# Kernel optimization log

Measured on AMD Instinct MI355X. Metric: run time of the kernel, lower is better.

## Reference

```python
import jax, jax.numpy as jnp
import numpy as np

B, S, H, L, NH, DH, V, FF, WD, W = 16, 512, 768, 12, 12, 64, 30522, 3072, 256, 255
T = S - 1


def layer_norm(x, s, b, eps=1e-12):
    m = jnp.mean(x, -1, keepdims=True)
    v = jnp.mean((x - m) ** 2, -1, keepdims=True)
    return (x - m) * jax.lax.rsqrt(v + eps) * s + b


def setup_inputs() -> dict:
    key = jax.random.key(0)
    ks = jax.random.split(key, 20)
    rng = np.random.RandomState(0)
    # ragged structure: words per sentence and wordpieces per word
    sent_lens = rng.randint(128, W + 1, size=B)
    token_lens = np.zeros((B, W), dtype=np.int32)
    for i in range(B):
        token_lens[i, : sent_lens[i]] = rng.randint(1, 3, size=sent_lens[i])
    bert_len = token_lens.sum(1)  # wordpieces per sentence (no CLS/SEP)
    attention_mask = (np.arange(S)[None, :] < (bert_len + 2)[:, None]).astype(np.int32)
    input_ids = rng.randint(0, V, size=(B, S)).astype(np.int32)
    sd = 0.02
    rn = lambda k, sh: jax.random.normal(k, sh, jnp.float32) * sd
    inp = {
        "input_ids": jnp.asarray(input_ids),
        "attention_mask": jnp.asarray(attention_mask),
        "token_lens": jnp.asarray(token_lens),
        "word_emb": rn(ks[0], (V, H)),
        "pos_emb": rn(ks[1], (S, H)),
        "type_emb": rn(ks[2], (2, H)),
        "emb_ln_s": jnp.ones((H,), jnp.float32),
        "emb_ln_b": jnp.zeros((H,), jnp.float32),
        "Wq": rn(ks[3], (L, H, H)), "bq": jnp.zeros((L, H), jnp.float32),
        "Wk": rn(ks[4], (L, H, H)), "bk": jnp.zeros((L, H), jnp.float32),
        "Wv": rn(ks[5], (L, H, H)), "bv": jnp.zeros((L, H), jnp.float32),
        "Wo": rn(ks[6], (L, H, H)), "bo": jnp.zeros((L, H), jnp.float32),
        "ln1_s": jnp.ones((L, H), jnp.float32), "ln1_b": jnp.zeros((L, H), jnp.float32),
        "W1": rn(ks[7], (L, H, FF)), "b1": jnp.zeros((L, FF), jnp.float32),
        "W2": rn(ks[8], (L, FF, H)), "b2": jnp.zeros((L, H), jnp.float32),
        "ln2_s": jnp.ones((L, H), jnp.float32), "ln2_b": jnp.zeros((L, H), jnp.float32),
        "proj_W": rn(ks[9], (H, WD)), "proj_b": jnp.zeros((WD,), jnp.float32),
    }
    return inp


def reference(input_ids, attention_mask, token_lens, word_emb, pos_emb, type_emb,
              emb_ln_s, emb_ln_b, Wq, bq, Wk, bk, Wv, bv, Wo, bo, ln1_s, ln1_b,
              W1, b1, W2, b2, ln2_s, ln2_b, proj_W, proj_b):
    # --- BERT embeddings ---
    h = word_emb[input_ids] + pos_emb[None, :, :] + type_emb[0][None, None, :]
    h = layer_norm(h, emb_ln_s, emb_ln_b)
    att_bias = (1.0 - attention_mask.astype(jnp.float32))[:, None, None, :] * -10000.0

    def block(h, p):
        wq, bq_, wk, bk_, wv, bv_, wo, bo_, l1s, l1b, w1, b1_, w2, b2_, l2s, l2b = p
        q = (h @ wq + bq_).reshape(B, S, NH, DH)
        k = (h @ wk + bk_).reshape(B, S, NH, DH)
        v = (h @ wv + bv_).reshape(B, S, NH, DH)
        scores = jnp.einsum('bqnd,bknd->bnqk', q, k) / np.float32(np.sqrt(DH)) + att_bias
        a = jax.nn.softmax(scores, axis=-1)
        ctx = jnp.einsum('bnqk,bknd->bqnd', a, v).reshape(B, S, H)
        h = layer_norm(h + ctx @ wo + bo_, l1s, l1b)
        f = jax.nn.gelu(h @ w1 + b1_, approximate=False) @ w2 + b2_
        h = layer_norm(h + f, l2s, l2b)
        return h, None

    h, _ = jax.lax.scan(block, h, (Wq, bq, Wk, bk, Wv, bv, Wo, bo, ln1_s, ln1_b,
                                   W1, b1, W2, b2, ln2_s, ln2_b))
    # drop [CLS], project to word_dims
    hid = h[:, 1:, :] @ proj_W + proj_b  # [B, T, WD]
    # --- ragged segment-mean merge (vectorized form of merge_embedding) ---
    cum = jnp.cumsum(token_lens, axis=1)  # [B, W]
    pos = jnp.arange(T)
    word_id = jnp.sum(pos[None, :, None] >= cum[:, None, :], axis=-1)  # token -> word
    valid = pos[None, :] < cum[:, -1][:, None]  # token within bert_len
    onehot = ((word_id[:, :, None] == jnp.arange(W)[None, None, :]) & valid[:, :, None]).astype(hid.dtype)
    sums = jnp.einsum('btw,btd->bwd', onehot, hid)  # [B, W, WD]
    means = sums / jnp.maximum(token_lens, 1)[:, :, None].astype(hid.dtype)
    word_masks = (token_lens > 0).astype(jnp.float32)  # [B, W]
    return means, word_masks
```

## Files before the change

### kernel.cpp

```cpp
#include <hip/hip_runtime.h>
#include <stdint.h>

#define B_ 16
#define S_ 512
#define H_ 768
#define L_ 12
#define NH_ 12
#define DH_ 64
#define FF_ 3072
#define WD_ 256
#define W_ 255
#define MTOK_ (B_*S_)
#define QKVN_ 2304
#define MPADR_ 128

typedef _Float16 f16;
typedef _Float16 f16x8 __attribute__((ext_vector_type(8)));
typedef _Float16 f16x4 __attribute__((ext_vector_type(4)));
typedef _Float16 f16x2 __attribute__((ext_vector_type(2)));
typedef float f32x4 __attribute__((ext_vector_type(4)));

#define SCHED_FENCE() __builtin_amdgcn_sched_barrier(0)

__device__ __forceinline__ float gelu_fast(float x) {
  float u = x * (1.0f + 0.044715f * x * x);
  float e = __expf(-1.5957691216f * u);
  return __fdividef(x, 1.0f + e);
}

__device__ __forceinline__ void gload16(const f16* g, f16* l) {
  __builtin_amdgcn_global_load_lds(
      (const __attribute__((address_space(1))) void*)g,
      (__attribute__((address_space(3))) void*)l, 16, 0, 0);
}

template<int BM, int BN, int ACT, int OUTF16, int BIAS, int QKVW, int SPLITK, int CIN, int COUT>
__global__ __launch_bounds__(256) void gemm2_k(
    const f16* __restrict__ A, const f16* __restrict__ Bm, void* __restrict__ Cv,
    const float* __restrict__ bias, f16* __restrict__ vTp,
    const int* __restrict__ rowmap, const int* __restrict__ meta,
    int lda, int ldb, int ldc, int K, float scale, long czoff)
{
  constexpr int MI = BM / 32;
  constexpr int NI = BN / 32;
  const int gx = gridDim.x;
  int flat = blockIdx.y * gx + blockIdx.x;
  const int nlive = (meta[1] / BM) * gx;
  if (flat >= nlive) return;
  {
    int q = nlive >> 3, r = nlive & 7;
    int xcd = flat & 7, idx = flat >> 3;
    flat = (xcd < r ? xcd * (q + 1) : r * (q + 1) + (xcd - r) * q) + idx;
  }
  const int row0 = (flat / gx) * BM;
  const int col0 = (flat % gx) * BN;
  const int z = (SPLITK > 1) ? blockIdx.z : 0;
  const int kc_len = K / SPLITK;
  A  += (size_t)z * kc_len;
  Bm += (size_t)z * kc_len;

  __shared__ __align__(16) f16 lA[BM * 64];
  __shared__ __align__(16) f16 lB[BN * 64];
  const int lane = threadIdx.x & 63;
  const int wave = threadIdx.x >> 6;
  const int wr = wave >> 1, wc = wave & 1;
  const int srow = lane >> 3;
  const int scol = lane & 7;
  const int cs = scol ^ srow;

  int arow[BM / 32];
#pragma unroll
  for (int i = 0; i < BM / 32; ++i) {
    int cr = row0 + (wave * (BM / 32) + i) * 8 + srow;
    arow[i] = CIN ? cr : rowmap[cr];
  }

  f32x4 acc[MI][NI] = {};
  const int nt = kc_len >> 6;
  const int rl = lane & 15, g = lane >> 4;
  for (int t = 0; t < nt; ++t) {
    __syncthreads();
    const int k0 = t * 64;
#pragma unroll
    for (int i = 0; i < BM / 32; ++i) {
      int seg = wave * (BM / 32) + i;
      gload16(&A[(size_t)arow[i] * lda + k0 + cs * 8], &lA[seg * 512]);
    }
#pragma unroll
    for (int i = 0; i < BN / 32; ++i) {
      int seg = wave * (BN / 32) + i;
      gload16(&Bm[(size_t)(col0 + seg * 8 + srow) * ldb + k0 + cs * 8], &lB[seg * 512]);
    }
    __syncthreads();
#pragma unroll
    for (int c = 0; c < 2; ++c) {
      f16x8 af[MI], bf[NI];
#pragma unroll
      for (int mi = 0; mi < MI; ++mi) {
        int r = wr * (MI * 16) + mi * 16 + rl;
        int u = (c * 4 + g) ^ (r & 7);
        af[mi] = *(const f16x8*)&lA[r * 64 + u * 8];
      }
#pragma unroll
      for (int ni = 0; ni < NI; ++ni) {
        int r = wc * (NI * 16) + ni * 16 + rl;
        int u = (c * 4 + g) ^ (r & 7);
        bf[ni] = *(const f16x8*)&lB[r * 64 + u * 8];
      }
#pragma unroll
      for (int mi = 0; mi < MI; ++mi)
#pragma unroll
        for (int ni = 0; ni < NI; ++ni)
          acc[mi][ni] = __builtin_amdgcn_mfma_f32_16x16x32_f16(af[mi], bf[ni], acc[mi][ni], 0, 0, 0);
    }
  }
  const int cl = lane & 15;
  const int rq = (lane >> 4) * 4;
#pragma unroll
  for (int mi = 0; mi < MI; ++mi) {
    const int crow0 = row0 + wr * (MI * 16) + mi * 16 + rq;
    int rows[4];
    bool contig;
    if constexpr (COUT && !QKVW) {
#pragma unroll
      for (int r = 0; r < 4; ++r) rows[r] = crow0 + r;
      contig = true;
    } else {
      const int4 rm4 = *(const int4*)&rowmap[crow0];
      rows[0] = rm4.x; rows[1] = rm4.y; rows[2] = rm4.z; rows[3] = rm4.w;
      contig = (rm4.w == rm4.x + 3) && ((rm4.x & 3) == 0);
    }
    (void)contig;
#pragma unroll
    for (int ni = 0; ni < NI; ++ni) {
      int col = col0 + wc * (NI * 16) + ni * 16 + cl;
      float bv = 0.f;
      if constexpr (BIAS) { if (SPLITK == 1 || z == 0) bv = bias[col]; }
      if constexpr (QKVW) {
        if (col >= 2 * H_) {
          int vc = col - 2 * H_;
          int h = vc >> 6, d = vc & 63;
          if (contig) {
            if (rows[0] < MTOK_) {
              int b = rows[0] >> 9, s = rows[0] & (S_ - 1);
              f16x4 o4;
#pragma unroll
              for (int r = 0; r < 4; ++r) o4[r] = (f16)(acc[mi][ni][r] * scale + bv);
              *(f16x4*)&vTp[(((size_t)(b * NH_ + h)) * DH_ + d) * S_ + s] = o4;
            }
          } else {
#pragma unroll
            for (int r = 0; r < 4; ++r) {
              int orow = rows[r];
              if (orow < MTOK_) {
                int b = orow >> 9, s = orow & (S_ - 1);
                vTp[(((size_t)(b * NH_ + h)) * DH_ + d) * S_ + s] = (f16)(acc[mi][ni][r] * scale + bv);
              }
            }
          }
          continue;
        }
      }
#pragma unroll
      for (int r = 0; r < 4; ++r) {
        float v = acc[mi][ni][r] * scale + bv;
        if constexpr (ACT == 1) v = gelu_fast(v);
        if constexpr (OUTF16) {
          ((f16*)Cv + (size_t)z * czoff)[(size_t)rows[r] * ldc + col] = (f16)v;
        } else {
          ((float*)Cv)[(size_t)rows[r] * ldc + col] = v;
        }
      }
    }
  }
}

__global__ __launch_bounds__(256) void fattn_k(
    const f16* __restrict__ qkv, const f16* __restrict__ vT,
    f16* __restrict__ ctx, const int* __restrict__ lenp)
{
  const int bh = blockIdx.x, qt = blockIdx.y;
  const int b = bh / NH_, h = bh - b * NH_;
  const int L = lenp[b];
  if ((qt << 6) >= L) return;
  const int nkt = (L + 63) >> 6;
  const int lane = threadIdx.x & 63, wave = threadIdx.x >> 6;
  const int rl = lane & 15, g = lane >> 4;
  const int srow = lane >> 3, scol = lane & 7;
  const int cs = scol ^ srow;

  __shared__ __align__(16) f16 lK[2][64 * 64];
  __shared__ __align__(16) f16 lV[2][64 * 64];
  __shared__ __align__(16) f16 lP[64 * 72];

  auto stage = [&](int p, int kt) {
#pragma unroll
    for (int i = 0; i < 2; ++i) {
      int seg = wave * 2 + i;
      int r = seg * 8 + srow;
      gload16(&qkv[((size_t)b * S_ + kt * 64 + r) * QKVN_ + H_ + h * DH_ + cs * 8], &lK[p][seg * 512]);
      gload16(&vT[((size_t)bh * DH_ + r) * S_ + kt * 64 + cs * 8], &lV[p][seg * 512]);
    }
  };

  const size_t qrow0 = (size_t)b * S_ + qt * 64 + wave * 16;
  f16x8 qf[2];
#pragma unroll
  for (int kc = 0; kc < 2; ++kc) {
    qf[kc] = *(const f16x8*)&qkv[(qrow0 + rl) * QKVN_ + h * DH_ + kc * 32 + g * 8];
    qf[kc] *= (f16)0.125f;
  }

  float lsum = 0.f;
  f32x4 accO[4] = {};

  stage(0, 0);
  for (int kt = 0; kt < nkt; ++kt) {
    if (kt + 1 < nkt) {
      stage((kt + 1) & 1, kt + 1);
      asm volatile("s_waitcnt vmcnt(4) lgkmcnt(0)" ::: "memory");
    } else {
      asm volatile("s_waitcnt vmcnt(0) lgkmcnt(0)" ::: "memory");
    }
    SCHED_FENCE();
    __builtin_amdgcn_s_barrier();
    SCHED_FENCE();
    const int p = kt & 1;

    f32x4 accS[4] = {};
    __builtin_amdgcn_s_setprio(1);
#pragma unroll
    for (int kc = 0; kc < 2; ++kc) {
#pragma unroll
      for (int ak = 0; ak < 4; ++ak) {
        int row = ak * 16 + rl;
        int u = (kc * 4 + g) ^ (row & 7);
        f16x8 kf = *(const f16x8*)&lK[p][row * 64 + u * 8];
        accS[ak] = __builtin_amdgcn_mfma_f32_16x16x32_f16(kf, qf[kc], accS[ak], 0, 0, 0);
      }
    }
    __builtin_amdgcn_s_setprio(0);

    const int kvb = kt * 64 + g * 4;
    {
      float pv[16];
      float ps = 0.f;
#pragma unroll
      for (int ak = 0; ak < 4; ++ak)
#pragma unroll
        for (int r = 0; r < 4; ++r) {
          float pp = (kvb + ak * 16 + r < L) ? __expf(accS[ak][r]) : 0.f;
          pv[ak * 4 + r] = pp;
          ps += pp;
        }
      ps += __shfl_xor(ps, 16);
      ps += __shfl_xor(ps, 32);
      lsum += ps;
      const int qrow = wave * 16 + rl;
#pragma unroll
      for (int ak = 0; ak < 4; ++ak)
#pragma unroll
        for (int r2 = 0; r2 < 2; ++r2) {
          f16x2 pk = { (f16)pv[ak * 4 + r2 * 2], (f16)pv[ak * 4 + r2 * 2 + 1] };
          *(f16x2*)&lP[qrow * 72 + ak * 16 + g * 4 + r2 * 2] = pk;
        }
    }
    __builtin_amdgcn_s_setprio(1);
#pragma unroll
    for (int kc = 0; kc < 2; ++kc) {
      f16x8 pa = *(const f16x8*)&lP[(wave * 16 + rl) * 72 + kc * 32 + g * 8];
      f16x8 vf[4];
#pragma unroll
      for (int bd = 0; bd < 4; ++bd) {
        int vrow = bd * 16 + rl;
        int u = (kc * 4 + g) ^ (vrow & 7);
        vf[bd] = *(const f16x8*)&lV[p][vrow * 64 + u * 8];
      }
#pragma unroll
      for (int bd = 0; bd < 4; ++bd)
        accO[bd] = __builtin_amdgcn_mfma_f32_16x16x32_f16(pa, vf[bd], accO[bd], 0, 0, 0);
    }
    __builtin_amdgcn_s_setprio(0);
    SCHED_FENCE();
    asm volatile("s_waitcnt lgkmcnt(0)" ::: "memory");
    SCHED_FENCE();
    __builtin_amdgcn_s_barrier();
    SCHED_FENCE();
  }

  float linv = 1.f / lsum;
  const size_t orow0 = (size_t)b * S_ + qt * 64 + wave * 16;
#pragma unroll
  for (int r = 0; r < 4; ++r) {
    float li = __shfl(linv, (lane & 48) | (g * 4 + r));
    int q = g * 4 + r;
#pragma unroll
    for (int bd = 0; bd < 4; ++bd)
      ctx[(orow0 + q) * H_ + h * DH_ + bd * 16 + rl] = (f16)(accO[bd][r] * li);
  }
}

template<typename TI>
__global__ __launch_bounds__(256) void transpose_f16_k(
    const TI* __restrict__ in, f16* __restrict__ out,
    int ldin, int ldout, long i1, long o1)
{
  const int z = blockIdx.z;
  in  += (size_t)z * i1;
  out += (size_t)z * o1;
  __shared__ float t[32][33];
  const int kt = blockIdx.y * 32, nt = blockIdx.x * 32;
  const int tx = threadIdx.x & 31, tg = threadIdx.x >> 5;
#pragma unroll
  for (int i = 0; i < 4; ++i) {
    int k = tg * 4 + i;
    t[k][tx] = (float)in[(size_t)(kt + k) * ldin + nt + tx];
  }
  __syncthreads();
#pragma unroll
  for (int i = 0; i < 4; ++i) {
    int n = tg * 4 + i;
    out[(size_t)(nt + n) * ldout + kt + tx] = (f16)t[tx][n];
  }
}

__global__ void bias_cat_k(const float* __restrict__ bq, const float* __restrict__ bk,
                           const float* __restrict__ bv, float* __restrict__ out) {
  const int l = blockIdx.y;
  const int j = blockIdx.x * 256 + threadIdx.x;
  float v = (j < H_) ? bq[l * H_ + j] : (j < 2 * H_) ? bk[l * H_ + j - H_] : bv[l * H_ + j - 2 * H_];
  out[l * QKVN_ + j] = v;
}

__global__ __launch_bounds__(256) void embed_ln_k(
    const int* __restrict__ ids, const float* __restrict__ wemb,
    const float* __restrict__ pemb, const float* __restrict__ temb,
    const float* __restrict__ lns, const float* __restrict__ lnb,
    f16* __restrict__ h16)
{
  const int row = blockIdx.x * 4 + (threadIdx.x >> 6);
  const int lane = threadIdx.x & 63;
  const int s = row & (S_ - 1);
  const float4* wp = (const float4*)(wemb + (size_t)ids[row] * H_);
  const float4* pp = (const float4*)(pemb + (size_t)s * H_);
  const float4* tp = (const float4*)temb;
  float4 x[3]; float sm = 0.f, sq = 0.f;
#pragma unroll
  for (int j = 0; j < 3; ++j) {
    int i4 = lane + 64 * j;
    float4 a = wp[i4], bb = pp[i4], c = tp[i4];
    float4 v; v.x = a.x + bb.x + c.x; v.y = a.y + bb.y + c.y;
    v.z = a.z + bb.z + c.z; v.w = a.w + bb.w + c.w;
    x[j] = v;
    sm += v.x + v.y + v.z + v.w;
    sq += v.x * v.x + v.y * v.y + v.z * v.z + v.w * v.w;
  }
#pragma unroll
  for (int o = 32; o > 0; o >>= 1) { sm += __shfl_xor(sm, o); sq += __shfl_xor(sq, o); }
  float mean = sm * (1.f / H_);
  float inv = rsqrtf(sq * (1.f / H_) - mean * mean + 1e-12f);
  f16* ho = h16 + (size_t)row * H_;
#pragma unroll
  for (int j = 0; j < 3; ++j) {
    int i4 = lane + 64 * j;
    float4 sc = ((const float4*)lns)[i4], bi = ((const float4*)lnb)[i4];
    float4 v = x[j];
    f16x4 o4 = {(f16)((v.x - mean) * inv * sc.x + bi.x),
                (f16)((v.y - mean) * inv * sc.y + bi.y),
                (f16)((v.z - mean) * inv * sc.z + bi.z),
                (f16)((v.w - mean) * inv * sc.w + bi.w)};
    *(f16x4*)&ho[i4 * 4] = o4;
  }
}

__global__ __launch_bounds__(256) void ln_res_k(
    f16* __restrict__ h16, const f16* __restrict__ tmpA, const f16* __restrict__ tmpB,
    const float* __restrict__ lns, const float* __restrict__ lnb,
    const int* __restrict__ rowmap, const int* __restrict__ meta)
{
  const int crow = blockIdx.x * 4 + (threadIdx.x >> 6);
  if (crow >= meta[0]) return;
  const int row = rowmap[crow];
  const int lane = threadIdx.x & 63;
  const f16x4* hp = (const f16x4*)(h16 + (size_t)row * H_);
  const f16x4* ta = (const f16x4*)(tmpA + (size_t)crow * H_);
  const f16x4* tb = (const f16x4*)(tmpB + (size_t)crow * H_);
  float4 x[3]; float sm = 0.f, sq = 0.f;
#pragma unroll
  for (int j = 0; j < 3; ++j) {
    int i4 = lane + 64 * j;
    f16x4 a = hp[i4], va = ta[i4], vb = tb[i4];
    float4 v;
    v.x = (float)a[0] + (float)va[0] + (float)vb[0];
    v.y = (float)a[1] + (float)va[1] + (float)vb[1];
    v.z = (float)a[2] + (float)va[2] + (float)vb[2];
    v.w = (float)a[3] + (float)va[3] + (float)vb[3];
    x[j] = v;
    sm += v.x + v.y + v.z + v.w;
    sq += v.x * v.x + v.y * v.y + v.z * v.z + v.w * v.w;
  }
#pragma unroll
  for (int o = 32; o > 0; o >>= 1) { sm += __shfl_xor(sm, o); sq += __shfl_xor(sq, o); }
  float mean = sm * (1.f / H_);
  float inv = rsqrtf(sq * (1.f / H_) - mean * mean + 1e-12f);
  f16* ho = h16 + (size_t)row * H_;
#pragma unroll
  for (int j = 0; j < 3; ++j) {
    int i4 = lane + 64 * j;
    float4 sc = ((const float4*)lns)[i4], bi = ((const float4*)lnb)[i4];
    float4 v = x[j];
    f16x4 o4 = {(f16)((v.x - mean) * inv * sc.x + bi.x),
                (f16)((v.y - mean) * inv * sc.y + bi.y),
                (f16)((v.z - mean) * inv * sc.z + bi.z),
                (f16)((v.w - mean) * inv * sc.w + bi.w)};
    *(f16x4*)&ho[i4 * 4] = o4;
  }
}

__global__ void lenmap_k(const int* __restrict__ mask, int* __restrict__ len,
                         int* __restrict__ meta, int* __restrict__ rowmap) {
  const int t = threadIdx.x;
  __shared__ int red[512];
  __shared__ int cum[17];
  const int b = t >> 5, sl = t & 31;
  int part = 0;
#pragma unroll
  for (int j = 0; j < 16; ++j) part += mask[b * S_ + sl + 32 * j];
  red[t] = part; __syncthreads();
  for (int o = 16; o > 0; o >>= 1) {
    if (sl < o) red[t] += red[t + o];
    __syncthreads();
  }
  if (t == 0) {
    int c = 0; cum[0] = 0;
    for (int bb = 0; bb < B_; ++bb) { len[bb] = red[bb * 32]; c += red[bb * 32]; cum[bb + 1] = c; }
    meta[0] = c;
    meta[1] = (c + 127) & ~127;
  }
  __syncthreads();
  const int Mv = cum[16];
  for (int i = t; i < MTOK_ + MPADR_; i += 512) {
    int orig;
    if (i < Mv) {
      int bb = 0;
#pragma unroll
      for (int k = 1; k <= 16; ++k) bb += (i >= cum[k]) ? 1 : 0;
      orig = bb * S_ + (i - cum[bb]);
    } else {
      int d = i - Mv;
      orig = MTOK_ + (d < MPADR_ ? d : MPADR_ - 1);
    }
    rowmap[i] = orig;
  }
}

__global__ __launch_bounds__(256) void merge_k(
    const f16* __restrict__ proj, const int* __restrict__ tl,
    float* __restrict__ means, float* __restrict__ masks)
{
  const int w = blockIdx.x, b = blockIdx.y;
  const int t = threadIdx.x;
  __shared__ int red[256];
  int part = 0;
  for (int j = t; j < w; j += 256) part += tl[b * W_ + j];
  red[t] = part; __syncthreads();
  for (int o = 128; o > 0; o >>= 1) { if (t < o) red[t] += red[t + o]; __syncthreads(); }
  const int start = red[0];
  const int len = tl[b * W_ + w];
  float s = 0.f;
  for (int l = 0; l < len; ++l)
    s += (float)proj[((size_t)b * S_ + 1 + start + l) * WD_ + t];
  means[((size_t)b * W_ + w) * WD_ + t] = (len > 0) ? s / (float)len : 0.f;
  if (t == 0) masks[b * W_ + w] = (len > 0) ? 1.f : 0.f;
}

extern "C" void kernel_launch(void* const* d_in, const int* in_sizes, int n_in,
                              void* d_out, int out_size, void* d_ws, size_t ws_size,
                              hipStream_t stream)
{
  (void)in_sizes; (void)n_in; (void)out_size;
  const int*   ids   = (const int*)d_in[0];
  const int*   amask = (const int*)d_in[1];
  const int*   tlens = (const int*)d_in[2];
  const float* wemb  = (const float*)d_in[3];
  const float* pemb  = (const float*)d_in[4];
  const float* temb  = (const float*)d_in[5];
  const float* elns  = (const float*)d_in[6];
  const float* elnb  = (const float*)d_in[7];
  const float* Wq = (const float*)d_in[8];  const float* bq = (const float*)d_in[9];
  const float* Wk = (const float*)d_in[10]; const float* bk = (const float*)d_in[11];
  const float* Wv = (const float*)d_in[12]; const float* bv = (const float*)d_in[13];
  const float* Wo = (const float*)d_in[14]; const float* bo = (const float*)d_in[15];
  const float* l1s = (const float*)d_in[16]; const float* l1b = (const float*)d_in[17];
  const float* W1 = (const float*)d_in[18]; const float* b1 = (const float*)d_in[19];
  const float* W2 = (const float*)d_in[20]; const float* b2 = (const float*)d_in[21];
  const float* l2s = (const float*)d_in[22]; const float* l2b = (const float*)d_in[23];
  const float* pW = (const float*)d_in[24]; const float* pb = (const float*)d_in[25];

  const int MR = MTOK_ + MPADR_;
  char* ws = (char*)d_ws;
  size_t off = 0;
  auto alloc = [&](size_t n) { void* r = ws + off; off += (n + 255) & ~(size_t)255; return r; };
  f16*   h16   = (f16*)alloc((size_t)MR * H_ * 2);
  f16*   qkv   = (f16*)alloc((size_t)MR * QKVN_ * 2);
  f16*   ctx16 = (f16*)alloc((size_t)MR * H_ * 2);
  f16*   vT    = (f16*)alloc((size_t)B_ * NH_ * DH_ * S_ * 2);
  f16*   ff16  = (f16*)alloc((size_t)MR * FF_ * 2);
  f16*   tmp16 = (f16*)alloc((size_t)MR * H_ * 2 * 2);
  f16*   projf = (f16*)alloc((size_t)MR * WD_ * 2);
  f16*   pwT   = (f16*)alloc((size_t)WD_ * H_ * 2);
  float* bqkv  = (float*)alloc((size_t)L_ * QKVN_ * 4);
  int*   lenb  = (int*)alloc(256);
  int*   meta  = (int*)alloc(256);
  int*   rowmap = (int*)alloc((size_t)MR * 4);
  f16*   tmp16b = tmp16 + (size_t)MR * H_;

  const size_t wqkv_sz = (size_t)QKVN_ * H_ * 2;
  const size_t wo_sz   = (size_t)H_ * H_ * 2;
  const size_t w1_sz   = (size_t)H_ * FF_ * 2;
  const size_t w2_sz   = (size_t)FF_ * H_ * 2;
  const size_t per_layer_w = wqkv_sz + wo_sz + w1_sz + w2_sz;
  const bool big = ws_size >= off + (size_t)L_ * per_layer_w + 8192;
  const int nz = big ? L_ : 1;
  f16* wqkv0 = (f16*)alloc((size_t)nz * wqkv_sz);
  f16* wo0   = (f16*)alloc((size_t)nz * wo_sz);
  f16* w10   = (f16*)alloc((size_t)nz * w1_sz);
  f16* w20   = (f16*)alloc((size_t)nz * w2_sz);

  lenmap_k<<<1, 512, 0, stream>>>(amask, lenb, meta, rowmap);
  embed_ln_k<<<MTOK_ / 4, 256, 0, stream>>>(ids, wemb, pemb, temb, elns, elnb, h16);
  transpose_f16_k<float><<<dim3(WD_/32, H_/32, 1), 256, 0, stream>>>(pW, pwT, WD_, H_, 0, 0);
  bias_cat_k<<<dim3(QKVN_/256, L_), 256, 0, stream>>>(bq, bk, bv, bqkv);

  if (big) {
    transpose_f16_k<float><<<dim3(H_/32, H_/32, L_), 256, 0, stream>>>(
        Wq, wqkv0,                   H_, H_, (long)H_*H_, (long)QKVN_*H_);
    transpose_f16_k<float><<<dim3(H_/32, H_/32, L_), 256, 0, stream>>>(
        Wk, wqkv0 + (size_t)H_*H_,   H_, H_, (long)H_*H_, (long)QKVN_*H_);
    transpose_f16_k<float><<<dim3(H_/32, H_/32, L_), 256, 0, stream>>>(
        Wv, wqkv0 + (size_t)2*H_*H_, H_, H_, (long)H_*H_, (long)QKVN_*H_);
    transpose_f16_k<float><<<dim3(H_/32, H_/32, L_), 256, 0, stream>>>(
        Wo, wo0, H_, H_, (long)H_*H_, (long)H_*H_);
    transpose_f16_k<float><<<dim3(FF_/32, H_/32, L_), 256, 0, stream>>>(
        W1, w10, FF_, H_, (long)H_*FF_, (long)H_*FF_);
    transpose_f16_k<float><<<dim3(H_/32, FF_/32, L_), 256, 0, stream>>>(
        W2, w20, H_, FF_, (long)FF_*H_, (long)FF_*H_);
  }

  for (int l = 0; l < L_; ++l) {
    f16* wqkv_l = wqkv0 + (size_t)(big ? l : 0) * QKVN_ * H_;
    f16* wo_l   = wo0   + (size_t)(big ? l : 0) * H_ * H_;
    f16* w1_l   = w10   + (size_t)(big ? l : 0) * H_ * FF_;
    f16* w2_l   = w20   + (size_t)(big ? l : 0) * FF_ * H_;
    if (!big) {
      transpose_f16_k<float><<<dim3(H_/32, H_/32, 1), 256, 0, stream>>>(
          Wq + (size_t)l*H_*H_, wqkv_l,                   H_, H_, 0, 0);
      transpose_f16_k<float><<<dim3(H_/32, H_/32, 1), 256, 0, stream>>>(
          Wk + (size_t)l*H_*H_, wqkv_l + (size_t)H_*H_,   H_, H_, 0, 0);
      transpose_f16_k<float><<<dim3(H_/32, H_/32, 1), 256, 0, stream>>>(
          Wv + (size_t)l*H_*H_, wqkv_l + (size_t)2*H_*H_, H_, H_, 0, 0);
      transpose_f16_k<float><<<dim3(H_/32, H_/32, 1), 256, 0, stream>>>(
          Wo + (size_t)l*H_*H_, wo_l, H_, H_, 0, 0);
      transpose_f16_k<float><<<dim3(FF_/32, H_/32, 1), 256, 0, stream>>>(
          W1 + (size_t)l*H_*FF_, w1_l, FF_, H_, 0, 0);
      transpose_f16_k<float><<<dim3(H_/32, FF_/32, 1), 256, 0, stream>>>(
          W2 + (size_t)l*FF_*H_, w2_l, H_, FF_, 0, 0);
    }
    gemm2_k<128,128,0,1,1,1,1,0,0><<<dim3(QKVN_/128, MTOK_/128, 1), 256, 0, stream>>>(
        h16, wqkv_l, qkv, bqkv + (size_t)l*QKVN_, vT, rowmap, meta, H_, H_, QKVN_, H_, 1.0f, 0);
    fattn_k<<<dim3(B_*NH_, S_/64), 256, 0, stream>>>(qkv, vT, ctx16, lenb);
    gemm2_k<64,64,0,1,1,0,2,0,1><<<dim3(H_/64, MTOK_/64, 2), 256, 0, stream>>>(
        ctx16, wo_l, tmp16, bo + (size_t)l*H_, nullptr, rowmap, meta, H_, H_, H_, H_, 1.0f, (long)MR * H_);
    ln_res_k<<<MTOK_/4, 256, 0, stream>>>(h16, tmp16, tmp16b, l1s + (size_t)l*H_, l1b + (size_t)l*H_, rowmap, meta);
    gemm2_k<128,128,1,1,1,0,1,0,1><<<dim3(FF_/128, MTOK_/128, 1), 256, 0, stream>>>(
        h16, w1_l, ff16, b1 + (size_t)l*FF_, nullptr, rowmap, meta, H_, H_, FF_, H_, 1.0f, 0);
    gemm2_k<64,64,0,1,1,0,2,1,1><<<dim3(H_/64, MTOK_/64, 2), 256, 0, stream>>>(
        ff16, w2_l, tmp16, b2 + (size_t)l*H_, nullptr, rowmap, meta, FF_, FF_, H_, FF_, 1.0f, (long)MR * H_);
    ln_res_k<<<MTOK_/4, 256, 0, stream>>>(h16, tmp16, tmp16b, l2s + (size_t)l*H_, l2b + (size_t)l*H_, rowmap, meta);
  }

  gemm2_k<64,64,0,1,1,0,1,0,0><<<dim3(WD_/64, MTOK_/64, 1), 256, 0, stream>>>(
      h16, pwT, projf, pb, nullptr, rowmap, meta, H_, H_, WD_, H_, 1.0f, 0);
  merge_k<<<dim3(W_, B_), 256, 0, stream>>>(projf, tlens,
      (float*)d_out, (float*)d_out + (size_t)B_ * W_ * WD_);
}
```

Before: 2.259 ms.

## Keep hidden states in compacted row layout across all layer kernels

Hidden states are now stored in compacted (valid-token-only) row order from the embedding onward, rather than in the padded B*S layout with a rowmap gather. GEMMs switch to a template mode that reads A rows contiguously, attention scatters its output through a new cmap into compacted rows, and layer norm and merge index compacted rows directly. The aim is to remove indirect row gathers and make A-operand loads contiguous, at the cost of an extra index map and a per-row indirection in the attention epilogue.

```diff
diff --git a/kernel.cpp b/kernel.cpp
--- a/kernel.cpp
+++ b/kernel.cpp
@@ -177,7 +177,7 @@
 
 __global__ __launch_bounds__(256) void fattn_k(
     const f16* __restrict__ qkv, const f16* __restrict__ vT,
-    f16* __restrict__ ctx, const int* __restrict__ lenp)
+    f16* __restrict__ ctx, const int* __restrict__ lenp, const int* __restrict__ cmap)
 {
   const int bh = blockIdx.x, qt = blockIdx.y;
   const int b = bh / NH_, h = bh - b * NH_;
@@ -289,14 +289,15 @@
   }
 
   float linv = 1.f / lsum;
-  const size_t orow0 = (size_t)b * S_ + qt * 64 + wave * 16;
+  const int orow0 = b * S_ + qt * 64 + wave * 16;
 #pragma unroll
   for (int r = 0; r < 4; ++r) {
     float li = __shfl(linv, (lane & 48) | (g * 4 + r));
     int q = g * 4 + r;
+    int crow = cmap[orow0 + q];
 #pragma unroll
     for (int bd = 0; bd < 4; ++bd)
-      ctx[(orow0 + q) * H_ + h * DH_ + bd * 16 + rl] = (f16)(accO[bd][r] * li);
+      ctx[(size_t)crow * H_ + h * DH_ + bd * 16 + rl] = (f16)(accO[bd][r] * li);
   }
 }
 
@@ -336,9 +337,11 @@
     const int* __restrict__ ids, const float* __restrict__ wemb,
     const float* __restrict__ pemb, const float* __restrict__ temb,
     const float* __restrict__ lns, const float* __restrict__ lnb,
-    f16* __restrict__ h16)
-{
-  const int row = blockIdx.x * 4 + (threadIdx.x >> 6);
+    f16* __restrict__ h16, const int* __restrict__ rowmap, const int* __restrict__ meta)
+{
+  const int crow = blockIdx.x * 4 + (threadIdx.x >> 6);
+  if (crow >= meta[0]) return;
+  const int row = rowmap[crow];
   const int lane = threadIdx.x & 63;
   const int s = row & (S_ - 1);
   const float4* wp = (const float4*)(wemb + (size_t)ids[row] * H_);
@@ -359,7 +362,7 @@
   for (int o = 32; o > 0; o >>= 1) { sm += __shfl_xor(sm, o); sq += __shfl_xor(sq, o); }
   float mean = sm * (1.f / H_);
   float inv = rsqrtf(sq * (1.f / H_) - mean * mean + 1e-12f);
-  f16* ho = h16 + (size_t)row * H_;
+  f16* ho = h16 + (size_t)crow * H_;
 #pragma unroll
   for (int j = 0; j < 3; ++j) {
     int i4 = lane + 64 * j;
@@ -376,13 +379,12 @@
 __global__ __launch_bounds__(256) void ln_res_k(
     f16* __restrict__ h16, const f16* __restrict__ tmpA, const f16* __restrict__ tmpB,
     const float* __restrict__ lns, const float* __restrict__ lnb,
-    const int* __restrict__ rowmap, const int* __restrict__ meta)
+    const int* __restrict__ meta)
 {
   const int crow = blockIdx.x * 4 + (threadIdx.x >> 6);
   if (crow >= meta[0]) return;
-  const int row = rowmap[crow];
   const int lane = threadIdx.x & 63;
-  const f16x4* hp = (const f16x4*)(h16 + (size_t)row * H_);
+  const f16x4* hp = (const f16x4*)(h16 + (size_t)crow * H_);
   const f16x4* ta = (const f16x4*)(tmpA + (size_t)crow * H_);
   const f16x4* tb = (const f16x4*)(tmpB + (size_t)crow * H_);
   float4 x[3]; float sm = 0.f, sq = 0.f;
@@ -403,7 +405,7 @@
   for (int o = 32; o > 0; o >>= 1) { sm += __shfl_xor(sm, o); sq += __shfl_xor(sq, o); }
   float mean = sm * (1.f / H_);
   float inv = rsqrtf(sq * (1.f / H_) - mean * mean + 1e-12f);
-  f16* ho = h16 + (size_t)row * H_;
+  f16* ho = h16 + (size_t)crow * H_;
 #pragma unroll
   for (int j = 0; j < 3; ++j) {
     int i4 = lane + 64 * j;
@@ -418,7 +420,8 @@
 }
 
 __global__ void lenmap_k(const int* __restrict__ mask, int* __restrict__ len,
-                         int* __restrict__ meta, int* __restrict__ rowmap) {
+                         int* __restrict__ meta, int* __restrict__ rowmap,
+                         int* __restrict__ cmap) {
   const int t = threadIdx.x;
   __shared__ int red[512];
   __shared__ int cum[17];
@@ -436,6 +439,7 @@
     for (int bb = 0; bb < B_; ++bb) { len[bb] = red[bb * 32]; c += red[bb * 32]; cum[bb + 1] = c; }
     meta[0] = c;
     meta[1] = (c + 127) & ~127;
+    for (int k = 0; k <= 16; ++k) meta[2 + k] = cum[k];
   }
   __syncthreads();
   const int Mv = cum[16];
@@ -452,10 +456,16 @@
     }
     rowmap[i] = orig;
   }
+  for (int i = t; i < MTOK_; i += 512) {
+    int bb = i >> 9, s = i & (S_ - 1);
+    int lb = cum[bb + 1] - cum[bb];
+    cmap[i] = (s < lb) ? (cum[bb] + s) : (Mv + (i & 127));
+  }
 }
 
 __global__ __launch_bounds__(256) void merge_k(
     const f16* __restrict__ proj, const int* __restrict__ tl,
+    const int* __restrict__ meta,
     float* __restrict__ means, float* __restrict__ masks)
 {
   const int w = blockIdx.x, b = blockIdx.y;
@@ -467,9 +477,10 @@
   for (int o = 128; o > 0; o >>= 1) { if (t < o) red[t] += red[t + o]; __syncthreads(); }
   const int start = red[0];
   const int len = tl[b * W_ + w];
+  const int base = meta[2 + b] + 1 + start;
   float s = 0.f;
   for (int l = 0; l < len; ++l)
-    s += (float)proj[((size_t)b * S_ + 1 + start + l) * WD_ + t];
+    s += (float)proj[((size_t)(base + l)) * WD_ + t];
   means[((size_t)b * W_ + w) * WD_ + t] = (len > 0) ? s / (float)len : 0.f;
   if (t == 0) masks[b * W_ + w] = (len > 0) ? 1.f : 0.f;
 }
@@ -513,6 +524,7 @@
   int*   lenb  = (int*)alloc(256);
   int*   meta  = (int*)alloc(256);
   int*   rowmap = (int*)alloc((size_t)MR * 4);
+  int*   cmap  = (int*)alloc((size_t)MTOK_ * 4);
   f16*   tmp16b = tmp16 + (size_t)MR * H_;
 
   const size_t wqkv_sz = (size_t)QKVN_ * H_ * 2;
@@ -527,8 +539,8 @@
   f16* w10   = (f16*)alloc((size_t)nz * w1_sz);
   f16* w20   = (f16*)alloc((size_t)nz * w2_sz);
 
-  lenmap_k<<<1, 512, 0, stream>>>(amask, lenb, meta, rowmap);
-  embed_ln_k<<<MTOK_ / 4, 256, 0, stream>>>(ids, wemb, pemb, temb, elns, elnb, h16);
+  lenmap_k<<<1, 512, 0, stream>>>(amask, lenb, meta, rowmap, cmap);
+  embed_ln_k<<<MTOK_ / 4, 256, 0, stream>>>(ids, wemb, pemb, temb, elns, elnb, h16, rowmap, meta);
   transpose_f16_k<float><<<dim3(WD_/32, H_/32, 1), 256, 0, stream>>>(pW, pwT, WD_, H_, 0, 0);
   bias_cat_k<<<dim3(QKVN_/256, L_), 256, 0, stream>>>(bq, bk, bv, bqkv);
 
@@ -566,21 +578,21 @@
       transpose_f16_k<float><<<dim3(H_/32, FF_/32, 1), 256, 0, stream>>>(
           W2 + (size_t)l*FF_*H_, w2_l, H_, FF_, 0, 0);
     }
-    gemm2_k<128,128,0,1,1,1,1,0,0><<<dim3(QKVN_/128, MTOK_/128, 1), 256, 0, stream>>>(
+    gemm2_k<128,128,0,1,1,1,1,1,0><<<dim3(QKVN_/128, MTOK_/128, 1), 256, 0, stream>>>(
         h16, wqkv_l, qkv, bqkv + (size_t)l*QKVN_, vT, rowmap, meta, H_, H_, QKVN_, H_, 1.0f, 0);
-    fattn_k<<<dim3(B_*NH_, S_/64), 256, 0, stream>>>(qkv, vT, ctx16, lenb);
-    gemm2_k<64,64,0,1,1,0,2,0,1><<<dim3(H_/64, MTOK_/64, 2), 256, 0, stream>>>(
+    fattn_k<<<dim3(B_*NH_, S_/64), 256, 0, stream>>>(qkv, vT, ctx16, lenb, cmap);
+    gemm2_k<64,64,0,1,1,0,2,1,1><<<dim3(H_/64, MTOK_/64, 2), 256, 0, stream>>>(
         ctx16, wo_l, tmp16, bo + (size_t)l*H_, nullptr, rowmap, meta, H_, H_, H_, H_, 1.0f, (long)MR * H_);
-    ln_res_k<<<MTOK_/4, 256, 0, stream>>>(h16, tmp16, tmp16b, l1s + (size_t)l*H_, l1b + (size_t)l*H_, rowmap, meta);
-    gemm2_k<128,128,1,1,1,0,1,0,1><<<dim3(FF_/128, MTOK_/128, 1), 256, 0, stream>>>(
+    ln_res_k<<<MTOK_/4, 256, 0, stream>>>(h16, tmp16, tmp16b, l1s + (size_t)l*H_, l1b + (size_t)l*H_, meta);
+    gemm2_k<128,128,1,1,1,0,1,1,1><<<dim3(FF_/128, MTOK_/128, 1), 256, 0, stream>>>(
         h16, w1_l, ff16, b1 + (size_t)l*FF_, nullptr, rowmap, meta, H_, H_, FF_, H_, 1.0f, 0);
     gemm2_k<64,64,0,1,1,0,2,1,1><<<dim3(H_/64, MTOK_/64, 2), 256, 0, stream>>>(
         ff16, w2_l, tmp16, b2 + (size_t)l*H_, nullptr, rowmap, meta, FF_, FF_, H_, FF_, 1.0f, (long)MR * H_);
-    ln_res_k<<<MTOK_/4, 256, 0, stream>>>(h16, tmp16, tmp16b, l2s + (size_t)l*H_, l2b + (size_t)l*H_, rowmap, meta);
-  }
-
-  gemm2_k<64,64,0,1,1,0,1,0,0><<<dim3(WD_/64, MTOK_/64, 1), 256, 0, stream>>>(
+    ln_res_k<<<MTOK_/4, 256, 0, stream>>>(h16, tmp16, tmp16b, l2s + (size_t)l*H_, l2b + (size_t)l*H_, meta);
+  }
+
+  gemm2_k<64,64,0,1,1,0,1,1,1><<<dim3(WD_/64, MTOK_/64, 1), 256, 0, stream>>>(
       h16, pwT, projf, pb, nullptr, rowmap, meta, H_, H_, WD_, H_, 1.0f, 0);
-  merge_k<<<dim3(W_, B_), 256, 0, stream>>>(projf, tlens,
+  merge_k<<<dim3(W_, B_), 256, 0, stream>>>(projf, tlens, meta,
       (float*)d_out, (float*)d_out + (size_t)B_ * W_ * WD_);
 }
```

Result: no change. 2.238 ms (-1.0%).
